# Performance work log

Hardware: AMD Instinct MI355X
Metric: run time of the kernel (lower is better)

## Reference

```python
import jax, jax.numpy as jnp
import numpy as np
from jax import lax

B, T_SRC, I, H, L, O = 1024, 1024, 64, 512, 64, 1


def _lstm_cell(x, h, c, W_ih, W_hh, b):
    # PyTorch gate order: i, f, g, o. b = b_ih + b_hh (same math).
    gates = x @ W_ih.T + h @ W_hh.T + b  # (B, 4H)
    i, f, g, o = jnp.split(gates, 4, axis=-1)
    c_new = jax.nn.sigmoid(f) * c + jax.nn.sigmoid(i) * jnp.tanh(g)
    h_new = jax.nn.sigmoid(o) * jnp.tanh(c_new)
    return h_new, c_new


def setup_inputs() -> dict:
    key = jax.random.key(0)
    ks = jax.random.split(key, 16)
    s_e = 1.0 / np.sqrt(H)
    inp = {
        "src": jax.random.normal(ks[0], (B, T_SRC, I), dtype=jnp.float32),
        "eps": jax.random.normal(ks[1], (B, L), dtype=jnp.float32),
        "tgt_len": 1024,
        # encoder LSTM
        "W_ih_e": jax.random.uniform(ks[2], (4 * H, I), jnp.float32, -s_e, s_e),
        "W_hh_e": jax.random.uniform(ks[3], (4 * H, H), jnp.float32, -s_e, s_e),
        "b_e": jax.random.uniform(ks[4], (4 * H,), jnp.float32, -s_e, s_e),
        # fc_mu / fc_logvar
        "W_mu": jax.random.uniform(ks[5], (L, H), jnp.float32, -s_e, s_e),
        "b_mu": jax.random.uniform(ks[6], (L,), jnp.float32, -s_e, s_e),
        "W_lv": jax.random.uniform(ks[7], (L, H), jnp.float32, -s_e, s_e),
        "b_lv": jax.random.uniform(ks[8], (L,), jnp.float32, -s_e, s_e),
        # z -> h0, c0
        "W_zh": jax.random.uniform(ks[9], (H, L), jnp.float32, -s_e, s_e),
        "b_zh": jax.random.uniform(ks[10], (H,), jnp.float32, -s_e, s_e),
        "W_zc": jax.random.uniform(ks[11], (H, L), jnp.float32, -s_e, s_e),
        "b_zc": jax.random.uniform(ks[12], (H,), jnp.float32, -s_e, s_e),
        # decoder LSTM + fc_out
        "W_ih_d": jax.random.uniform(ks[13], (4 * H, O), jnp.float32, -s_e, s_e),
        "W_hh_d": jax.random.uniform(ks[14], (4 * H, H), jnp.float32, -s_e, s_e),
        "b_d": jax.random.uniform(ks[15], (4 * H,), jnp.float32, -s_e, s_e),
        "W_out": jax.random.uniform(jax.random.fold_in(key, 100), (O, H), jnp.float32, -s_e, s_e),
        "b_out": jax.random.uniform(jax.random.fold_in(key, 101), (O,), jnp.float32, -s_e, s_e),
    }
    return inp


def reference(src, eps, W_ih_e, W_hh_e, b_e, W_mu, b_mu, W_lv, b_lv,
              W_zh, b_zh, W_zc, b_zc, W_ih_d, W_hh_d, b_d, W_out, b_out,
              tgt_len):
    batch = src.shape[0]
    hid = W_hh_e.shape[1]

    # ---- Encoder: LSTM over src, take final hidden state ----
    def enc_step(carry, x_t):
        h, c = carry
        h, c = _lstm_cell(x_t, h, c, W_ih_e, W_hh_e, b_e)
        return (h, c), None

    h0 = jnp.zeros((batch, hid), src.dtype)
    (h_n, _), _ = lax.scan(enc_step, (h0, h0), jnp.swapaxes(src, 0, 1))

    mu = h_n @ W_mu.T + b_mu          # (B, L)
    logvar = h_n @ W_lv.T + b_lv      # (B, L)

    # ---- Reparameterize ----
    z = mu + eps * jnp.exp(0.5 * logvar)

    h_d = jnp.tanh(z @ W_zh.T + b_zh)
    c_d = jnp.tanh(z @ W_zc.T + b_zc)
    x0 = jnp.zeros((batch, W_ih_d.shape[1]), src.dtype)  # (B, output_size)

    def dec_step(carry, _):
        h, c, x = carry
        h, c = _lstm_cell(x, h, c, W_ih_d, W_hh_d, b_d)
        out = h @ W_out.T + b_out     # (B, O)
        return (h, c, out), out

    _, outs = lax.scan(dec_step, (h_d, c_d, x0), None, length=tgt_len)
    recon = jnp.swapaxes(outs, 0, 1)  # (B, tgt_len, O)
    return recon, mu, logvar
```

## Files before the change

kernel.cpp:

```cpp
#include <hip/hip_runtime.h>


#define NWG  256
#define NTHR 256

typedef __attribute__((ext_vector_type(8))) short short8;
typedef __attribute__((ext_vector_type(4))) float f32x4;
typedef __attribute__((ext_vector_type(4))) unsigned int u32x4;

constexpr int Bt = 1024, Tt = 1024, In = 64, Hn = 512, Ln = 64;
constexpr int KE = In + Hn;
constexpr int BSE = KE + 8;
constexpr int KD = Hn;
constexpr int BSD = KD + 8;
constexpr int HSTn = 40;
constexpr int LDS_BYTES = 128 * BSE * 2 + 32 * HSTn * 2;

template<bool B> struct BoolC { static constexpr bool value = B; };

__device__ __forceinline__ float bf2f(unsigned short s){
  unsigned u = ((unsigned)s) << 16; float f; __builtin_memcpy(&f, &u, 4); return f;
}
__device__ __forceinline__ unsigned short f2bf(float f){
  unsigned u; __builtin_memcpy(&u, &f, 4);
  u += 0x7FFFu + ((u >> 16) & 1u);
  return (unsigned short)(u >> 16);
}
__device__ __forceinline__ float sigm(float x){ return 1.0f / (1.0f + __expf(-x)); }
__device__ __forceinline__ float tanh_(float x){ float e = __expf(2.0f * x); return 1.0f - 2.0f / (e + 1.0f); }

template<bool SAME, int OFF>
__device__ __forceinline__ u32x4 ldA(const void* p){
  u32x4 r;
  if constexpr (SAME) asm volatile("global_load_dwordx4 %0, %1, off offset:%c2 sc0" : "=&v"(r) : "v"(p), "i"(OFF));
  else                asm volatile("global_load_dwordx4 %0, %1, off offset:%c2 sc0 sc1" : "=&v"(r) : "v"(p), "i"(OFF));
  return r;
}
template<int OFF>
__device__ __forceinline__ u32x4 ldP(const void* p){
  u32x4 r;
  asm volatile("global_load_dwordx4 %0, %1, off offset:%c2" : "=&v"(r) : "v"(p), "i"(OFF));
  return r;
}
template<bool SAME>
__device__ __forceinline__ float ld32w(const void* p){
  float r;
  if constexpr (SAME) asm volatile("global_load_dword %0, %1, off sc0" : "=&v"(r) : "v"(p));
  else                asm volatile("global_load_dword %0, %1, off sc0 sc1" : "=&v"(r) : "v"(p));
  asm volatile("s_waitcnt vmcnt(0)" : "+v"(r));
  return r;
}
template<bool SAME>
__device__ __forceinline__ void st16x(void* p, unsigned v){
  if constexpr (SAME) asm volatile("global_store_short %0, %1, off sc0" :: "v"(p), "v"(v) : "memory");
  else                asm volatile("global_store_short %0, %1, off sc0 sc1" :: "v"(p), "v"(v) : "memory");
}
template<bool SAME>
__device__ __forceinline__ void st32x(void* p, float v){
  if constexpr (SAME) asm volatile("global_store_dword %0, %1, off sc0" :: "v"(p), "v"(v) : "memory");
  else                asm volatile("global_store_dword %0, %1, off sc0 sc1" :: "v"(p), "v"(v) : "memory");
}
template<bool SAME>
__device__ __forceinline__ void st128x(void* p, u32x4 v){
  if constexpr (SAME) asm volatile("global_store_dwordx4 %0, %1, off sc0" :: "v"(p), "v"(v) : "memory");
  else                asm volatile("global_store_dwordx4 %0, %1, off sc0 sc1" :: "v"(p), "v"(v) : "memory");
}
__device__ __forceinline__ void stP32(void* p, float v){
  asm volatile("global_store_dword %0, %1, off" :: "v"(p), "v"(v) : "memory");
}
__device__ __forceinline__ void atomAddF(float* p, float v){
  asm volatile("global_atomic_add_f32 %0, %1, off" :: "v"(p), "v"(v) : "memory");
}
__device__ __forceinline__ unsigned ldMall(const unsigned* p){
  unsigned r;
  asm volatile("global_load_dword %0, %1, off sc0 sc1" : "=&v"(r) : "v"(p) : "memory");
  asm volatile("s_waitcnt vmcnt(0)" : "+v"(r) :: "memory");
  return r;
}
__device__ __forceinline__ void stMall(unsigned* p, unsigned v){
  asm volatile("global_store_dword %0, %1, off sc0 sc1" :: "v"(p), "v"(v) : "memory");
}

__device__ __forceinline__ void release(unsigned* cnt){
  asm volatile("s_waitcnt vmcnt(0)" ::: "memory");
  __syncthreads();
  if (threadIdx.x == 0)
    __hip_atomic_fetch_add(cnt, 1u, __ATOMIC_RELAXED, __HIP_MEMORY_SCOPE_AGENT);
}
__device__ __forceinline__ void acquire(unsigned* cnt, unsigned target){
  if (threadIdx.x == 0 && target){
    int g = 0;
    while (__hip_atomic_load(cnt, __ATOMIC_RELAXED, __HIP_MEMORY_SCOPE_AGENT) < target){
      if (++g > (1 << 20)) break;
      __builtin_amdgcn_s_sleep(1);
    }
  }
  __syncthreads();
}

#define LOADC1(C, CB) do{                                  \
    A[C][0] = ldA<SAME, ((CB) +  0) * 2>(ap);              \
    A[C][1] = ldA<SAME, ((CB) + 32) * 2>(ap);              \
    A[C][2] = ldA<SAME, ((CB) + 64) * 2>(ap);              \
    A[C][3] = ldA<SAME, ((CB) + 96) * 2>(ap); }while(0)

#define TIE1(C) "+v"(A[C][0]), "+v"(A[C][1]), "+v"(A[C][2]), "+v"(A[C][3])
#define WAITC1(C, N) asm volatile("s_waitcnt vmcnt(" N ")" : TIE1(C))

#define COMPC1(C, K0, BS) do{                                                    \
    _Pragma("unroll") for (int ti_ = 0; ti_ < 4; ++ti_){                         \
      short8 a_ = __builtin_bit_cast(short8, A[C][ti_]);                         \
      _Pragma("unroll") for (int ni_ = 0; ni_ < 4; ++ni_){                       \
        short8 bv_ = *(const short8*)(bbase + ni_ * 16 * (BS) + (K0) + ti_ * 32);\
        acc[ni_] = __builtin_amdgcn_mfma_f32_16x16x32_bf16(a_, bv_, acc[ni_], 0, 0, 0); \
      } } }while(0)

extern "C" __global__ void __launch_bounds__(NTHR, 1)
vae_fused(const float* __restrict__ src, const float* __restrict__ eps,
          const float* __restrict__ Wih_e, const float* __restrict__ Whh_e, const float* __restrict__ b_e,
          const float* __restrict__ Wmu, const float* __restrict__ bmu,
          const float* __restrict__ Wlv, const float* __restrict__ blv,
          const float* __restrict__ Wzh, const float* __restrict__ bzh,
          const float* __restrict__ Wzc, const float* __restrict__ bzc,
          const float* __restrict__ Wih_d, const float* __restrict__ Whh_d, const float* __restrict__ b_d,
          const float* __restrict__ Wout, const float* __restrict__ bout,
          float* __restrict__ out,
          unsigned* cntF_all, unsigned* cntA_all, unsigned* cntB_all, unsigned* xcdbuf,
          unsigned short* hbuf0, unsigned short* hbuf1,
          float* zbuf, float* obuf)
{
  const int tid  = threadIdx.x;
  const int wg   = blockIdx.x;
  const int lane = tid & 63;
  const int wave = tid >> 6;
  const int wm   = wave >> 1, wn = wave & 1;
  const int mt   = wg & 15;
  const int nt   = wg >> 4;
  unsigned* cntF = cntF_all + mt * 16;
  unsigned* cntA = cntA_all + mt * 16;
  unsigned* cntB = cntB_all + mt * 16;
  unsigned barsF = 0;

  extern __shared__ short bpanel[];
  unsigned short* hst = (unsigned short*)(bpanel + 128 * BSE);

  const int l15 = lane & 15;
  const int l4  = lane >> 4;
  const int kq  = l4 * 8;
  const int jcol = nt * 32 + wn * 16 + l15;

  unsigned xcc;
  asm volatile("s_getreg_b32 %0, hwreg(HW_REG_XCC_ID)" : "=s"(xcc));
  if (tid == 0) stMall(xcdbuf + mt * 16 + nt, xcc + 1u);
  release(cntF); barsF += 16; acquire(cntF, barsF);
  unsigned vx = xcc + 1u;
  if (lane < 16) vx = ldMall(xcdbuf + mt * 16 + lane);
  const bool same_xcd = (__ballot(vx == xcc + 1u) == ~0ull);

  auto body = [&](auto SC){
    constexpr bool SAME = decltype(SC)::value;

    {
      const int idx = nt * NTHR + tid;
      const u32x4 z = {0u, 0u, 0u, 0u};
      st128x<SAME>(hbuf0 + (size_t)(mt * 64 + (idx >> 6)) * Hn + (idx & 63) * 8, z);
    }
    for (int idx = tid; idx < 128 * KE; idx += NTHR){
      int q = idx / KE;
      int k = idx - q * KE;
      int gate = (q >> 4) & 3, jl = q & 15, wnn = (q >> 6) & 1;
      int j = nt * 32 + wnn * 16 + jl;
      int r = gate * Hn + j;
      float w = (k < In) ? Wih_e[r * In + k] : Whh_e[(size_t)r * Hn + (k - In)];
      bpanel[q * BSE + k] = (short)f2bf(w);
    }
    float biasr[4], wihr[4];
    #pragma unroll
    for (int ni = 0; ni < 4; ++ni) biasr[ni] = b_e[ni * Hn + jcol];
    release(cntF); barsF += 16; acquire(cntF, barsF);

    float cA[4] = {0.f,0.f,0.f,0.f}, cB[4] = {0.f,0.f,0.f,0.f};
    const f32x4 fz = {0.f, 0.f, 0.f, 0.f};
    unsigned needA = 0, needB = 0;

    auto enc_phase = [&](int X, int t, unsigned* cntX, unsigned need, float (&cX)[4]){
      const int arow = mt * 64 + X * 32 + wm * 16 + l15;
      const unsigned short* hs = (t & 1) ? hbuf1 : hbuf0;
      unsigned short*       hd = (t & 1) ? hbuf0 : hbuf1;

      const float* sp = src + ((size_t)arow * Tt + t) * In + kq;
      u32x4 sv0 = ldP<0>(sp), sv1 = ldP<16>(sp), sv2 = ldP<128>(sp), sv3 = ldP<144>(sp);

      acquire(cntX, need);

      const unsigned short* ap = hs + (size_t)arow * Hn + kq;
      u32x4 A[4][4];
      LOADC1(0,   0); LOADC1(1, 128); LOADC1(2, 256); LOADC1(3, 384);

      asm volatile("s_waitcnt vmcnt(16)" : "+v"(sv0), "+v"(sv1), "+v"(sv2), "+v"(sv3));
      f32x4 f0 = __builtin_bit_cast(f32x4, sv0);
      f32x4 f1 = __builtin_bit_cast(f32x4, sv1);
      f32x4 f2 = __builtin_bit_cast(f32x4, sv2);
      f32x4 f3 = __builtin_bit_cast(f32x4, sv3);
      short8 sa0, sa1;
      #pragma unroll
      for (int e = 0; e < 4; ++e){
        sa0[e] = (short)f2bf(f0[e]); sa0[4 + e] = (short)f2bf(f1[e]);
        sa1[e] = (short)f2bf(f2[e]); sa1[4 + e] = (short)f2bf(f3[e]);
      }

      f32x4 acc[4] = {fz, fz, fz, fz};
      const short* bbase = bpanel + (wn * 64 + l15) * BSE + kq;
      #pragma unroll
      for (int ni = 0; ni < 4; ++ni){
        short8 bv0 = *(const short8*)(bbase + ni * 16 * BSE + 0);
        short8 bv1 = *(const short8*)(bbase + ni * 16 * BSE + 32);
        acc[ni] = __builtin_amdgcn_mfma_f32_16x16x32_bf16(sa0, bv0, acc[ni], 0, 0, 0);
        acc[ni] = __builtin_amdgcn_mfma_f32_16x16x32_bf16(sa1, bv1, acc[ni], 0, 0, 0);
      }

      WAITC1(0, "12"); COMPC1(0, In +   0, BSE);
      WAITC1(1,  "8"); COMPC1(1, In + 128, BSE);
      WAITC1(2,  "4"); COMPC1(2, In + 256, BSE);
      WAITC1(3,  "0"); COMPC1(3, In + 384, BSE);

      #pragma unroll
      for (int r = 0; r < 4; ++r){
        float gi = acc[0][r] + biasr[0];
        float gf = acc[1][r] + biasr[1];
        float gg = acc[2][r] + biasr[2];
        float go = acc[3][r] + biasr[3];
        float cn = sigm(gf) * cX[r] + sigm(gi) * tanh_(gg);
        cX[r] = cn;
        float hn = sigm(go) * tanh_(cn);
        hst[(wm * 16 + l4 * 4 + r) * HSTn + wn * 16 + l15] = f2bf(hn);
      }
      __syncthreads();
      if (tid < 128){
        u32x4 hv = *(const u32x4*)(hst + (tid >> 2) * HSTn + (tid & 3) * 8);
        st128x<SAME>(hd + (size_t)(mt * 64 + X * 32 + (tid >> 2)) * Hn + nt * 32 + (tid & 3) * 8, hv);
      }
      release(cntX);
    };

    for (int t = 0; t < Tt; ++t){
      enc_phase(0, t, cntA, needA, cA); needA += 16;
      enc_phase(1, t, cntB, needB, cB); needB += 16;
    }
    release(cntF); barsF += 16; acquire(cntF, barsF);

    {
      const int lt = nt * NTHR + tid;
      const int b  = mt * 64 + (lt >> 6);
      const int l  = lt & 63;
      const unsigned short* hp = hbuf0 + (size_t)b * Hn;
      const float* wmrow = Wmu + l * Hn;
      const float* wlrow = Wlv + l * Hn;
      float smu = 0.f, slv = 0.f;
      for (int jj = 0; jj < Hn; jj += 32){
        u32x4 v0 = ldA<SAME,0>(hp + jj),  v1 = ldA<SAME,16>(hp + jj);
        u32x4 v2 = ldA<SAME,32>(hp + jj), v3 = ldA<SAME,48>(hp + jj);
        asm volatile("s_waitcnt vmcnt(0)" : "+v"(v0), "+v"(v1), "+v"(v2), "+v"(v3));
        short8 h0 = __builtin_bit_cast(short8, v0);
        short8 h1 = __builtin_bit_cast(short8, v1);
        short8 h2 = __builtin_bit_cast(short8, v2);
        short8 h3 = __builtin_bit_cast(short8, v3);
        #pragma unroll
        for (int e = 0; e < 8; ++e){
          float g0 = bf2f((unsigned short)h0[e]), g1 = bf2f((unsigned short)h1[e]);
          float g2 = bf2f((unsigned short)h2[e]), g3 = bf2f((unsigned short)h3[e]);
          smu = __builtin_fmaf(g0, wmrow[jj + e], smu);      slv = __builtin_fmaf(g0, wlrow[jj + e], slv);
          smu = __builtin_fmaf(g1, wmrow[jj + 8 + e], smu);  slv = __builtin_fmaf(g1, wlrow[jj + 8 + e], slv);
          smu = __builtin_fmaf(g2, wmrow[jj + 16 + e], smu); slv = __builtin_fmaf(g2, wlrow[jj + 16 + e], slv);
          smu = __builtin_fmaf(g3, wmrow[jj + 24 + e], smu); slv = __builtin_fmaf(g3, wlrow[jj + 24 + e], slv);
        }
      }
      smu += bmu[l]; slv += blv[l];
      out[(size_t)Bt * Tt + (size_t)b * Ln + l] = smu;
      out[(size_t)Bt * Tt + (size_t)Bt * Ln + (size_t)b * Ln + l] = slv;
      st32x<SAME>(zbuf + (size_t)b * Ln + l, smu + eps[(size_t)b * Ln + l] * __expf(0.5f * slv));
    }
    release(cntF); barsF += 16; acquire(cntF, barsF);

    for (int idx = tid; idx < 128 * KD; idx += NTHR){
      int q = idx >> 9, k = idx & 511;
      int gate = (q >> 4) & 3, jl = q & 15, wnn = (q >> 6) & 1;
      int j = nt * 32 + wnn * 16 + jl;
      bpanel[q * BSD + k] = (short)f2bf(Whh_d[(size_t)(gate * Hn + j) * Hn + k]);
    }
    #pragma unroll
    for (int ni = 0; ni < 4; ++ni){
      biasr[ni] = b_d[ni * Hn + jcol];
      wihr[ni]  = Wih_d[ni * Hn + jcol];
    }
    const float woutr = Wout[jcol];
    const float bov   = bout[0];

    auto dec_init = [&](int X, float (&cX)[4]){
      #pragma unroll
      for (int r = 0; r < 4; ++r){
        int b = mt * 64 + X * 32 + wm * 16 + l4 * 4 + r;
        const float* zp  = zbuf + (size_t)b * Ln;
        const float* whr = Wzh + jcol * Ln;
        const float* wcr = Wzc + jcol * Ln;
        float sh = bzh[jcol], sc = bzc[jcol];
        for (int e0 = 0; e0 < Ln; e0 += 16){
          u32x4 z0 = ldA<SAME,0>(zp + e0),  z1 = ldA<SAME,16>(zp + e0);
          u32x4 z2 = ldA<SAME,32>(zp + e0), z3 = ldA<SAME,48>(zp + e0);
          asm volatile("s_waitcnt vmcnt(0)" : "+v"(z0), "+v"(z1), "+v"(z2), "+v"(z3));
          f32x4 zf0 = __builtin_bit_cast(f32x4, z0);
          f32x4 zf1 = __builtin_bit_cast(f32x4, z1);
          f32x4 zf2 = __builtin_bit_cast(f32x4, z2);
          f32x4 zf3 = __builtin_bit_cast(f32x4, z3);
          #pragma unroll
          for (int e = 0; e < 4; ++e){
            sh = __builtin_fmaf(zf0[e], whr[e0 + e], sh);      sc = __builtin_fmaf(zf0[e], wcr[e0 + e], sc);
            sh = __builtin_fmaf(zf1[e], whr[e0 + 4 + e], sh);  sc = __builtin_fmaf(zf1[e], wcr[e0 + 4 + e], sc);
            sh = __builtin_fmaf(zf2[e], whr[e0 + 8 + e], sh);  sc = __builtin_fmaf(zf2[e], wcr[e0 + 8 + e], sc);
            sh = __builtin_fmaf(zf3[e], whr[e0 + 12 + e], sh); sc = __builtin_fmaf(zf3[e], wcr[e0 + 12 + e], sc);
          }
        }
        cX[r] = tanh_(sc);
        st16x<SAME>(hbuf0 + (size_t)b * Hn + jcol, (unsigned)f2bf(tanh_(sh)));
      }
    };
    dec_init(0, cA);
    dec_init(1, cB);
    if (nt == 0 && tid < 3 * 64)
      st32x<SAME>(obuf + (tid >> 6) * Bt + mt * 64 + (tid & 63), bov);
    release(cntF); barsF += 16; acquire(cntF, barsF);

    auto dec_phase = [&](int X, int t, unsigned* cntX, unsigned need, float (&cX)[4]){
      const int arow = mt * 64 + X * 32 + wm * 16 + l15;
      const int brow = mt * 64 + X * 32 + wm * 16 + l4 * 4;
      const int rX0  = mt * 64 + X * 32;
      const unsigned short* hs = (t & 1) ? hbuf1 : hbuf0;
      unsigned short*       hd = (t & 1) ? hbuf0 : hbuf1;
      float*       oacc  = obuf + (t % 3) * Bt;
      const float* oread = obuf + ((t + 2) % 3) * Bt;
      float*       orst  = obuf + ((t + 1) % 3) * Bt;

      acquire(cntX, need);

      if (nt == 0){
        if (t > 0 && tid < 32){
          float w = ld32w<SAME>(oread + rX0 + tid);
          stP32(out + (size_t)(rX0 + tid) * Tt + (t - 1), w);
        }
        if (tid < 32) st32x<SAME>(orst + rX0 + tid, bov);
      }

      u32x4 xvv = ldA<SAME, 0>(oread + brow);
      const unsigned short* ap = hs + (size_t)arow * Hn + kq;
      u32x4 A[4][4];
      LOADC1(0,   0); LOADC1(1, 128); LOADC1(2, 256); LOADC1(3, 384);

      f32x4 acc[4] = {fz, fz, fz, fz};
      const short* bbase = bpanel + (wn * 64 + l15) * BSD + kq;
      WAITC1(0, "12"); COMPC1(0,   0, BSD);
      WAITC1(1,  "8"); COMPC1(1, 128, BSD);
      WAITC1(2,  "4"); COMPC1(2, 256, BSD);
      WAITC1(3,  "0"); COMPC1(3, 384, BSD);
      asm volatile("s_waitcnt vmcnt(0)" : "+v"(xvv));
      f32x4 xf = __builtin_bit_cast(f32x4, xvv);

      #pragma unroll
      for (int r = 0; r < 4; ++r){
        float x = (t == 0) ? 0.f : xf[r];
        float gi = acc[0][r] + biasr[0] + x * wihr[0];
        float gf = acc[1][r] + biasr[1] + x * wihr[1];
        float gg = acc[2][r] + biasr[2] + x * wihr[2];
        float go = acc[3][r] + biasr[3] + x * wihr[3];
        float cn = sigm(gf) * cX[r] + sigm(gi) * tanh_(gg);
        cX[r] = cn;
        float hn = sigm(go) * tanh_(cn);
        hst[(wm * 16 + l4 * 4 + r) * HSTn + wn * 16 + l15] = f2bf(hn);
        float pv = hn * woutr;
        pv += __shfl_xor(pv, 1);
        pv += __shfl_xor(pv, 2);
        pv += __shfl_xor(pv, 4);
        pv += __shfl_xor(pv, 8);
        if (l15 == 0) atomAddF(&oacc[brow + r], pv);
      }
      __syncthreads();
      if (tid < 128){
        u32x4 hv = *(const u32x4*)(hst + (tid >> 2) * HSTn + (tid & 3) * 8);
        st128x<SAME>(hd + (size_t)(mt * 64 + X * 32 + (tid >> 2)) * Hn + nt * 32 + (tid & 3) * 8, hv);
      }
      release(cntX);
    };

    for (int t = 0; t < Tt; ++t){
      dec_phase(0, t, cntA, needA, cA); needA += 16;
      dec_phase(1, t, cntB, needB, cB); needB += 16;
    }
    release(cntF); barsF += 16; acquire(cntF, barsF);

    if (nt == 0 && tid < 64){
      float w = ld32w<SAME>(obuf + 0 * Bt + mt * 64 + tid);
      stP32(out + (size_t)(mt * 64 + tid) * Tt + (Tt - 1), w);
    }
  };

  if (same_xcd) body(BoolC<true>{});
  else          body(BoolC<false>{});
}

extern "C" void kernel_launch(void* const* d_in, const int* in_sizes, int n_in,
                              void* d_out, int out_size, void* d_ws, size_t ws_size,
                              hipStream_t stream){
  (void)in_sizes; (void)n_in; (void)out_size; (void)ws_size;
  const float* src   = (const float*)d_in[0];
  const float* eps   = (const float*)d_in[1];
  const float* Wih_e = (const float*)d_in[3];
  const float* Whh_e = (const float*)d_in[4];
  const float* b_e   = (const float*)d_in[5];
  const float* Wmu   = (const float*)d_in[6];
  const float* bmu   = (const float*)d_in[7];
  const float* Wlv   = (const float*)d_in[8];
  const float* blv   = (const float*)d_in[9];
  const float* Wzh   = (const float*)d_in[10];
  const float* bzh   = (const float*)d_in[11];
  const float* Wzc   = (const float*)d_in[12];
  const float* bzc   = (const float*)d_in[13];
  const float* Wih_d = (const float*)d_in[14];
  const float* Whh_d = (const float*)d_in[15];
  const float* b_d   = (const float*)d_in[16];
  const float* Wout  = (const float*)d_in[17];
  const float* bout  = (const float*)d_in[18];

  char* ws = (char*)d_ws;
  unsigned*       cntF  = (unsigned*)ws;
  unsigned*       cntA  = (unsigned*)(ws + 1024);
  unsigned*       cntB  = (unsigned*)(ws + 2048);
  unsigned*       xcdb  = (unsigned*)(ws + 3072);
  unsigned short* h0    = (unsigned short*)(ws + 4096);
  unsigned short* h1    = (unsigned short*)(ws + 4096 + 1048576);
  float*          zbuf  = (float*)(ws + 4096 + 2 * 1048576);
  float*          obuf  = (float*)(ws + 4096 + 2 * 1048576 + 262144);

  hipFuncSetAttribute((const void*)vae_fused,
                      hipFuncAttributeMaxDynamicSharedMemorySize, LDS_BYTES);
  (void)hipMemsetAsync(ws, 0, 4096, stream);
  hipLaunchKernelGGL(vae_fused, dim3(NWG), dim3(NTHR), LDS_BYTES, stream,
                     src, eps, Wih_e, Whh_e, b_e, Wmu, bmu, Wlv, blv,
                     Wzh, bzh, Wzc, bzc, Wih_d, Whh_d, b_d, Wout, bout,
                     (float*)d_out, cntF, cntA, cntB, xcdb, h0, h1, zbuf, obuf);
}
```

Baseline: 17.93 ms.

## Double block size to process both 32-row halves concurrently with one barrier per step

Workgroups grow from 256 to 512 threads, so the 8 waves cover all 64 batch rows of a tile in one pass instead of alternating two 32-row halves with separate counters. Each timestep now does a single group barrier over one counter rather than two split-phase acquire/release pairs, and the spin-wait timeout is dropped. The decoder's float atomic add also gets an sc1 variant when the group spans XCDs. The cost is that the old overlap between one half's compute and the other half's barrier wait is lost. Register pressure per thread also rises under the new launch bounds.

```diff
diff --git a/kernel.cpp b/kernel.cpp
--- a/kernel.cpp
+++ b/kernel.cpp
@@ -2,7 +2,7 @@
 
 
 #define NWG  256
-#define NTHR 256
+#define NTHR 512
 
 typedef __attribute__((ext_vector_type(8))) short short8;
 typedef __attribute__((ext_vector_type(4))) float f32x4;
@@ -13,8 +13,8 @@
 constexpr int BSE = KE + 8;
 constexpr int KD = Hn;
 constexpr int BSD = KD + 8;
-constexpr int HSTn = 40;
-constexpr int LDS_BYTES = 128 * BSE * 2 + 32 * HSTn * 2;
+constexpr int HST = 40;
+constexpr int LDS_BYTES = 128 * BSE * 2 + 64 * HST * 2;
 
 template<bool B> struct BoolC { static constexpr bool value = B; };
 
@@ -68,8 +68,10 @@
 __device__ __forceinline__ void stP32(void* p, float v){
   asm volatile("global_store_dword %0, %1, off" :: "v"(p), "v"(v) : "memory");
 }
+template<bool SAME>
 __device__ __forceinline__ void atomAddF(float* p, float v){
-  asm volatile("global_atomic_add_f32 %0, %1, off" :: "v"(p), "v"(v) : "memory");
+  if constexpr (SAME) asm volatile("global_atomic_add_f32 %0, %1, off" :: "v"(p), "v"(v) : "memory");
+  else                asm volatile("global_atomic_add_f32 %0, %1, off sc1" :: "v"(p), "v"(v) : "memory");
 }
 __device__ __forceinline__ unsigned ldMall(const unsigned* p){
   unsigned r;
@@ -81,19 +83,13 @@
   asm volatile("global_store_dword %0, %1, off sc0 sc1" :: "v"(p), "v"(v) : "memory");
 }
 
-__device__ __forceinline__ void release(unsigned* cnt){
+__device__ __forceinline__ void group_sync(unsigned* cnt, unsigned target){
   asm volatile("s_waitcnt vmcnt(0)" ::: "memory");
   __syncthreads();
-  if (threadIdx.x == 0)
+  if (threadIdx.x == 0){
     __hip_atomic_fetch_add(cnt, 1u, __ATOMIC_RELAXED, __HIP_MEMORY_SCOPE_AGENT);
-}
-__device__ __forceinline__ void acquire(unsigned* cnt, unsigned target){
-  if (threadIdx.x == 0 && target){
-    int g = 0;
-    while (__hip_atomic_load(cnt, __ATOMIC_RELAXED, __HIP_MEMORY_SCOPE_AGENT) < target){
-      if (++g > (1 << 20)) break;
+    while (__hip_atomic_load(cnt, __ATOMIC_RELAXED, __HIP_MEMORY_SCOPE_AGENT) < target)
       __builtin_amdgcn_s_sleep(1);
-    }
   }
   __syncthreads();
 }
@@ -115,7 +111,7 @@
         acc[ni_] = __builtin_amdgcn_mfma_f32_16x16x32_bf16(a_, bv_, acc[ni_], 0, 0, 0); \
       } } }while(0)
 
-extern "C" __global__ void __launch_bounds__(NTHR, 1)
+extern "C" __global__ void __launch_bounds__(NTHR, 2)
 vae_fused(const float* __restrict__ src, const float* __restrict__ eps,
           const float* __restrict__ Wih_e, const float* __restrict__ Whh_e, const float* __restrict__ b_e,
           const float* __restrict__ Wmu, const float* __restrict__ bmu,
@@ -125,7 +121,7 @@
           const float* __restrict__ Wih_d, const float* __restrict__ Whh_d, const float* __restrict__ b_d,
           const float* __restrict__ Wout, const float* __restrict__ bout,
           float* __restrict__ out,
-          unsigned* cntF_all, unsigned* cntA_all, unsigned* cntB_all, unsigned* xcdbuf,
+          unsigned* cnt_all, unsigned* xcdbuf,
           unsigned short* hbuf0, unsigned short* hbuf1,
           float* zbuf, float* obuf)
 {
@@ -133,26 +129,27 @@
   const int wg   = blockIdx.x;
   const int lane = tid & 63;
   const int wave = tid >> 6;
-  const int wm   = wave >> 1, wn = wave & 1;
+  const int wm   = wave >> 1;
+  const int wn   = wave & 1;
   const int mt   = wg & 15;
   const int nt   = wg >> 4;
-  unsigned* cntF = cntF_all + mt * 16;
-  unsigned* cntA = cntA_all + mt * 16;
-  unsigned* cntB = cntB_all + mt * 16;
-  unsigned barsF = 0;
+  unsigned* cnt  = cnt_all + mt * 32;
+  unsigned bars  = 0;
 
   extern __shared__ short bpanel[];
   unsigned short* hst = (unsigned short*)(bpanel + 128 * BSE);
 
-  const int l15 = lane & 15;
-  const int l4  = lane >> 4;
-  const int kq  = l4 * 8;
-  const int jcol = nt * 32 + wn * 16 + l15;
+  const int l15   = lane & 15;
+  const int l4    = lane >> 4;
+  const int kq    = l4 * 8;
+  const int jcol  = nt * 32 + wn * 16 + l15;
+  const int arow0 = mt * 64 + wm * 16 + l15;
+  const int brow0 = mt * 64 + wm * 16 + l4 * 4;
 
   unsigned xcc;
   asm volatile("s_getreg_b32 %0, hwreg(HW_REG_XCC_ID)" : "=s"(xcc));
   if (tid == 0) stMall(xcdbuf + mt * 16 + nt, xcc + 1u);
-  release(cntF); barsF += 16; acquire(cntF, barsF);
+  bars += 16; group_sync(cnt, bars);
   unsigned vx = xcc + 1u;
   if (lane < 16) vx = ldMall(xcdbuf + mt * 16 + lane);
   const bool same_xcd = (__ballot(vx == xcc + 1u) == ~0ull);
@@ -162,8 +159,10 @@
 
     {
       const int idx = nt * NTHR + tid;
-      const u32x4 z = {0u, 0u, 0u, 0u};
-      st128x<SAME>(hbuf0 + (size_t)(mt * 64 + (idx >> 6)) * Hn + (idx & 63) * 8, z);
+      if (idx < 4096){
+        const u32x4 z = {0u, 0u, 0u, 0u};
+        st128x<SAME>(hbuf0 + (size_t)(mt * 64 + (idx >> 6)) * Hn + (idx & 63) * 8, z);
+      }
     }
     for (int idx = tid; idx < 128 * KE; idx += NTHR){
       int q = idx / KE;
@@ -177,24 +176,20 @@
     float biasr[4], wihr[4];
     #pragma unroll
     for (int ni = 0; ni < 4; ++ni) biasr[ni] = b_e[ni * Hn + jcol];
-    release(cntF); barsF += 16; acquire(cntF, barsF);
-
-    float cA[4] = {0.f,0.f,0.f,0.f}, cB[4] = {0.f,0.f,0.f,0.f};
+    bars += 16; group_sync(cnt, bars);
+
+    float c[4] = {0.f, 0.f, 0.f, 0.f};
     const f32x4 fz = {0.f, 0.f, 0.f, 0.f};
-    unsigned needA = 0, needB = 0;
-
-    auto enc_phase = [&](int X, int t, unsigned* cntX, unsigned need, float (&cX)[4]){
-      const int arow = mt * 64 + X * 32 + wm * 16 + l15;
+    u32x4 A[4][4];
+
+    for (int t = 0; t < Tt; ++t){
       const unsigned short* hs = (t & 1) ? hbuf1 : hbuf0;
       unsigned short*       hd = (t & 1) ? hbuf0 : hbuf1;
 
-      const float* sp = src + ((size_t)arow * Tt + t) * In + kq;
+      const float* sp = src + ((size_t)arow0 * Tt + t) * In + kq;
       u32x4 sv0 = ldP<0>(sp), sv1 = ldP<16>(sp), sv2 = ldP<128>(sp), sv3 = ldP<144>(sp);
 
-      acquire(cntX, need);
-
-      const unsigned short* ap = hs + (size_t)arow * Hn + kq;
-      u32x4 A[4][4];
+      const unsigned short* ap = hs + (size_t)arow0 * Hn + kq;
       LOADC1(0,   0); LOADC1(1, 128); LOADC1(2, 256); LOADC1(3, 384);
 
       asm volatile("s_waitcnt vmcnt(16)" : "+v"(sv0), "+v"(sv1), "+v"(sv2), "+v"(sv3));
@@ -230,57 +225,54 @@
         float gf = acc[1][r] + biasr[1];
         float gg = acc[2][r] + biasr[2];
         float go = acc[3][r] + biasr[3];
-        float cn = sigm(gf) * cX[r] + sigm(gi) * tanh_(gg);
-        cX[r] = cn;
+        float cn = sigm(gf) * c[r] + sigm(gi) * tanh_(gg);
+        c[r] = cn;
         float hn = sigm(go) * tanh_(cn);
-        hst[(wm * 16 + l4 * 4 + r) * HSTn + wn * 16 + l15] = f2bf(hn);
+        hst[(wm * 16 + l4 * 4 + r) * HST + wn * 16 + l15] = f2bf(hn);
       }
       __syncthreads();
-      if (tid < 128){
-        u32x4 hv = *(const u32x4*)(hst + (tid >> 2) * HSTn + (tid & 3) * 8);
-        st128x<SAME>(hd + (size_t)(mt * 64 + X * 32 + (tid >> 2)) * Hn + nt * 32 + (tid & 3) * 8, hv);
-      }
-      release(cntX);
-    };
-
-    for (int t = 0; t < Tt; ++t){
-      enc_phase(0, t, cntA, needA, cA); needA += 16;
-      enc_phase(1, t, cntB, needB, cB); needB += 16;
-    }
-    release(cntF); barsF += 16; acquire(cntF, barsF);
+      if (tid < 256){
+        int row = tid >> 2, sub = tid & 3;
+        u32x4 hv = *(const u32x4*)(hst + row * HST + sub * 8);
+        st128x<SAME>(hd + (size_t)(mt * 64 + row) * Hn + nt * 32 + sub * 8, hv);
+      }
+      bars += 16; group_sync(cnt, bars);
+    }
 
     {
       const int lt = nt * NTHR + tid;
-      const int b  = mt * 64 + (lt >> 6);
-      const int l  = lt & 63;
-      const unsigned short* hp = hbuf0 + (size_t)b * Hn;
-      const float* wmrow = Wmu + l * Hn;
-      const float* wlrow = Wlv + l * Hn;
-      float smu = 0.f, slv = 0.f;
-      for (int jj = 0; jj < Hn; jj += 32){
-        u32x4 v0 = ldA<SAME,0>(hp + jj),  v1 = ldA<SAME,16>(hp + jj);
-        u32x4 v2 = ldA<SAME,32>(hp + jj), v3 = ldA<SAME,48>(hp + jj);
-        asm volatile("s_waitcnt vmcnt(0)" : "+v"(v0), "+v"(v1), "+v"(v2), "+v"(v3));
-        short8 h0 = __builtin_bit_cast(short8, v0);
-        short8 h1 = __builtin_bit_cast(short8, v1);
-        short8 h2 = __builtin_bit_cast(short8, v2);
-        short8 h3 = __builtin_bit_cast(short8, v3);
-        #pragma unroll
-        for (int e = 0; e < 8; ++e){
-          float g0 = bf2f((unsigned short)h0[e]), g1 = bf2f((unsigned short)h1[e]);
-          float g2 = bf2f((unsigned short)h2[e]), g3 = bf2f((unsigned short)h3[e]);
-          smu = __builtin_fmaf(g0, wmrow[jj + e], smu);      slv = __builtin_fmaf(g0, wlrow[jj + e], slv);
-          smu = __builtin_fmaf(g1, wmrow[jj + 8 + e], smu);  slv = __builtin_fmaf(g1, wlrow[jj + 8 + e], slv);
-          smu = __builtin_fmaf(g2, wmrow[jj + 16 + e], smu); slv = __builtin_fmaf(g2, wlrow[jj + 16 + e], slv);
-          smu = __builtin_fmaf(g3, wmrow[jj + 24 + e], smu); slv = __builtin_fmaf(g3, wlrow[jj + 24 + e], slv);
+      if (lt < 4096){
+        const int b  = mt * 64 + (lt >> 6);
+        const int l  = lt & 63;
+        const unsigned short* hp = hbuf0 + (size_t)b * Hn;
+        const float* wmrow = Wmu + l * Hn;
+        const float* wlrow = Wlv + l * Hn;
+        float smu = 0.f, slv = 0.f;
+        for (int jj = 0; jj < Hn; jj += 32){
+          u32x4 v0 = ldA<SAME,0>(hp + jj),  v1 = ldA<SAME,16>(hp + jj);
+          u32x4 v2 = ldA<SAME,32>(hp + jj), v3 = ldA<SAME,48>(hp + jj);
+          asm volatile("s_waitcnt vmcnt(0)" : "+v"(v0), "+v"(v1), "+v"(v2), "+v"(v3));
+          short8 h0 = __builtin_bit_cast(short8, v0);
+          short8 h1 = __builtin_bit_cast(short8, v1);
+          short8 h2 = __builtin_bit_cast(short8, v2);
+          short8 h3 = __builtin_bit_cast(short8, v3);
+          #pragma unroll
+          for (int e = 0; e < 8; ++e){
+            float g0 = bf2f((unsigned short)h0[e]), g1 = bf2f((unsigned short)h1[e]);
+            float g2 = bf2f((unsigned short)h2[e]), g3 = bf2f((unsigned short)h3[e]);
+            smu = __builtin_fmaf(g0, wmrow[jj + e], smu);      slv = __builtin_fmaf(g0, wlrow[jj + e], slv);
+            smu = __builtin_fmaf(g1, wmrow[jj + 8 + e], smu);  slv = __builtin_fmaf(g1, wlrow[jj + 8 + e], slv);
+            smu = __builtin_fmaf(g2, wmrow[jj + 16 + e], smu); slv = __builtin_fmaf(g2, wlrow[jj + 16 + e], slv);
+            smu = __builtin_fmaf(g3, wmrow[jj + 24 + e], smu); slv = __builtin_fmaf(g3, wlrow[jj + 24 + e], slv);
+          }
         }
-      }
-      smu += bmu[l]; slv += blv[l];
-      out[(size_t)Bt * Tt + (size_t)b * Ln + l] = smu;
-      out[(size_t)Bt * Tt + (size_t)Bt * Ln + (size_t)b * Ln + l] = slv;
-      st32x<SAME>(zbuf + (size_t)b * Ln + l, smu + eps[(size_t)b * Ln + l] * __expf(0.5f * slv));
-    }
-    release(cntF); barsF += 16; acquire(cntF, barsF);
+        smu += bmu[l]; slv += blv[l];
+        out[(size_t)Bt * Tt + (size_t)b * Ln + l] = smu;
+        out[(size_t)Bt * Tt + (size_t)Bt * Ln + (size_t)b * Ln + l] = slv;
+        st32x<SAME>(zbuf + (size_t)b * Ln + l, smu + eps[(size_t)b * Ln + l] * __expf(0.5f * slv));
+      }
+    }
+    bars += 16; group_sync(cnt, bars);
 
     for (int idx = tid; idx < 128 * KD; idx += NTHR){
       int q = idx >> 9, k = idx & 511;
@@ -295,64 +287,53 @@
     }
     const float woutr = Wout[jcol];
     const float bov   = bout[0];
-
-    auto dec_init = [&](int X, float (&cX)[4]){
-      #pragma unroll
-      for (int r = 0; r < 4; ++r){
-        int b = mt * 64 + X * 32 + wm * 16 + l4 * 4 + r;
-        const float* zp  = zbuf + (size_t)b * Ln;
-        const float* whr = Wzh + jcol * Ln;
-        const float* wcr = Wzc + jcol * Ln;
-        float sh = bzh[jcol], sc = bzc[jcol];
-        for (int e0 = 0; e0 < Ln; e0 += 16){
-          u32x4 z0 = ldA<SAME,0>(zp + e0),  z1 = ldA<SAME,16>(zp + e0);
-          u32x4 z2 = ldA<SAME,32>(zp + e0), z3 = ldA<SAME,48>(zp + e0);
-          asm volatile("s_waitcnt vmcnt(0)" : "+v"(z0), "+v"(z1), "+v"(z2), "+v"(z3));
-          f32x4 zf0 = __builtin_bit_cast(f32x4, z0);
-          f32x4 zf1 = __builtin_bit_cast(f32x4, z1);
-          f32x4 zf2 = __builtin_bit_cast(f32x4, z2);
-          f32x4 zf3 = __builtin_bit_cast(f32x4, z3);
-          #pragma unroll
-          for (int e = 0; e < 4; ++e){
-            sh = __builtin_fmaf(zf0[e], whr[e0 + e], sh);      sc = __builtin_fmaf(zf0[e], wcr[e0 + e], sc);
-            sh = __builtin_fmaf(zf1[e], whr[e0 + 4 + e], sh);  sc = __builtin_fmaf(zf1[e], wcr[e0 + 4 + e], sc);
-            sh = __builtin_fmaf(zf2[e], whr[e0 + 8 + e], sh);  sc = __builtin_fmaf(zf2[e], wcr[e0 + 8 + e], sc);
-            sh = __builtin_fmaf(zf3[e], whr[e0 + 12 + e], sh); sc = __builtin_fmaf(zf3[e], wcr[e0 + 12 + e], sc);
-          }
+    #pragma unroll
+    for (int r = 0; r < 4; ++r){
+      int b = brow0 + r;
+      const float* zp  = zbuf + (size_t)b * Ln;
+      const float* whr = Wzh + jcol * Ln;
+      const float* wcr = Wzc + jcol * Ln;
+      float sh = bzh[jcol], sc = bzc[jcol];
+      for (int e0 = 0; e0 < Ln; e0 += 16){
+        u32x4 z0 = ldA<SAME,0>(zp + e0),  z1 = ldA<SAME,16>(zp + e0);
+        u32x4 z2 = ldA<SAME,32>(zp + e0), z3 = ldA<SAME,48>(zp + e0);
+        asm volatile("s_waitcnt vmcnt(0)" : "+v"(z0), "+v"(z1), "+v"(z2), "+v"(z3));
+        f32x4 zf0 = __builtin_bit_cast(f32x4, z0);
+        f32x4 zf1 = __builtin_bit_cast(f32x4, z1);
+        f32x4 zf2 = __builtin_bit_cast(f32x4, z2);
+        f32x4 zf3 = __builtin_bit_cast(f32x4, z3);
+        #pragma unroll
+        for (int e = 0; e < 4; ++e){
+          sh = __builtin_fmaf(zf0[e], whr[e0 + e], sh);      sc = __builtin_fmaf(zf0[e], wcr[e0 + e], sc);
+          sh = __builtin_fmaf(zf1[e], whr[e0 + 4 + e], sh);  sc = __builtin_fmaf(zf1[e], wcr[e0 + 4 + e], sc);
+          sh = __builtin_fmaf(zf2[e], whr[e0 + 8 + e], sh);  sc = __builtin_fmaf(zf2[e], wcr[e0 + 8 + e], sc);
+          sh = __builtin_fmaf(zf3[e], whr[e0 + 12 + e], sh); sc = __builtin_fmaf(zf3[e], wcr[e0 + 12 + e], sc);
         }
-        cX[r] = tanh_(sc);
-        st16x<SAME>(hbuf0 + (size_t)b * Hn + jcol, (unsigned)f2bf(tanh_(sh)));
-      }
-    };
-    dec_init(0, cA);
-    dec_init(1, cB);
+      }
+      c[r] = tanh_(sc);
+      st16x<SAME>(hbuf0 + (size_t)b * Hn + jcol, (unsigned)f2bf(tanh_(sh)));
+    }
     if (nt == 0 && tid < 3 * 64)
       st32x<SAME>(obuf + (tid >> 6) * Bt + mt * 64 + (tid & 63), bov);
-    release(cntF); barsF += 16; acquire(cntF, barsF);
-
-    auto dec_phase = [&](int X, int t, unsigned* cntX, unsigned need, float (&cX)[4]){
-      const int arow = mt * 64 + X * 32 + wm * 16 + l15;
-      const int brow = mt * 64 + X * 32 + wm * 16 + l4 * 4;
-      const int rX0  = mt * 64 + X * 32;
+    bars += 16; group_sync(cnt, bars);
+
+    for (int t = 0; t < Tt; ++t){
       const unsigned short* hs = (t & 1) ? hbuf1 : hbuf0;
       unsigned short*       hd = (t & 1) ? hbuf0 : hbuf1;
       float*       oacc  = obuf + (t % 3) * Bt;
       const float* oread = obuf + ((t + 2) % 3) * Bt;
       float*       orst  = obuf + ((t + 1) % 3) * Bt;
 
-      acquire(cntX, need);
-
       if (nt == 0){
-        if (t > 0 && tid < 32){
-          float w = ld32w<SAME>(oread + rX0 + tid);
-          stP32(out + (size_t)(rX0 + tid) * Tt + (t - 1), w);
+        if (t > 0 && tid < 64){
+          float w = ld32w<SAME>(oread + mt * 64 + tid);
+          stP32(out + (size_t)(mt * 64 + tid) * Tt + (t - 1), w);
         }
-        if (tid < 32) st32x<SAME>(orst + rX0 + tid, bov);
-      }
-
-      u32x4 xvv = ldA<SAME, 0>(oread + brow);
-      const unsigned short* ap = hs + (size_t)arow * Hn + kq;
-      u32x4 A[4][4];
+        if (tid < 64) st32x<SAME>(orst + mt * 64 + tid, bov);
+      }
+
+      u32x4 xvv = ldA<SAME, 0>(oread + brow0);
+      const unsigned short* ap = hs + (size_t)arow0 * Hn + kq;
       LOADC1(0,   0); LOADC1(1, 128); LOADC1(2, 256); LOADC1(3, 384);
 
       f32x4 acc[4] = {fz, fz, fz, fz};
@@ -371,31 +352,25 @@
         float gf = acc[1][r] + biasr[1] + x * wihr[1];
         float gg = acc[2][r] + biasr[2] + x * wihr[2];
         float go = acc[3][r] + biasr[3] + x * wihr[3];
-        float cn = sigm(gf) * cX[r] + sigm(gi) * tanh_(gg);
-        cX[r] = cn;
+        float cn = sigm(gf) * c[r] + sigm(gi) * tanh_(gg);
+        c[r] = cn;
         float hn = sigm(go) * tanh_(cn);
-        hst[(wm * 16 + l4 * 4 + r) * HSTn + wn * 16 + l15] = f2bf(hn);
+        hst[(wm * 16 + l4 * 4 + r) * HST + wn * 16 + l15] = f2bf(hn);
         float pv = hn * woutr;
         pv += __shfl_xor(pv, 1);
         pv += __shfl_xor(pv, 2);
         pv += __shfl_xor(pv, 4);
         pv += __shfl_xor(pv, 8);
-        if (l15 == 0) atomAddF(&oacc[brow + r], pv);
+        if (l15 == 0) atomAddF<SAME>(&oacc[brow0 + r], pv);
       }
       __syncthreads();
-      if (tid < 128){
-        u32x4 hv = *(const u32x4*)(hst + (tid >> 2) * HSTn + (tid & 3) * 8);
-        st128x<SAME>(hd + (size_t)(mt * 64 + X * 32 + (tid >> 2)) * Hn + nt * 32 + (tid & 3) * 8, hv);
-      }
-      release(cntX);
-    };
-
-    for (int t = 0; t < Tt; ++t){
-      dec_phase(0, t, cntA, needA, cA); needA += 16;
-      dec_phase(1, t, cntB, needB, cB); needB += 16;
-    }
-    release(cntF); barsF += 16; acquire(cntF, barsF);
-
+      if (tid < 256){
+        int row = tid >> 2, sub = tid & 3;
+        u32x4 hv = *(const u32x4*)(hst + row * HST + sub * 8);
+        st128x<SAME>(hd + (size_t)(mt * 64 + row) * Hn + nt * 32 + sub * 8, hv);
+      }
+      bars += 16; group_sync(cnt, bars);
+    }
     if (nt == 0 && tid < 64){
       float w = ld32w<SAME>(obuf + 0 * Bt + mt * 64 + tid);
       stP32(out + (size_t)(mt * 64 + tid) * Tt + (Tt - 1), w);
@@ -430,10 +405,8 @@
   const float* bout  = (const float*)d_in[18];
 
   char* ws = (char*)d_ws;
-  unsigned*       cntF  = (unsigned*)ws;
-  unsigned*       cntA  = (unsigned*)(ws + 1024);
-  unsigned*       cntB  = (unsigned*)(ws + 2048);
-  unsigned*       xcdb  = (unsigned*)(ws + 3072);
+  unsigned*       cnt   = (unsigned*)ws;
+  unsigned*       xcdb  = (unsigned*)(ws + 2048);
   unsigned short* h0    = (unsigned short*)(ws + 4096);
   unsigned short* h1    = (unsigned short*)(ws + 4096 + 1048576);
   float*          zbuf  = (float*)(ws + 4096 + 2 * 1048576);
@@ -445,5 +418,5 @@
   hipLaunchKernelGGL(vae_fused, dim3(NWG), dim3(NTHR), LDS_BYTES, stream,
                      src, eps, Wih_e, Whh_e, b_e, Wmu, bmu, Wlv, blv,
                      Wzh, bzh, Wzc, bzc, Wih_d, Whh_d, b_d, Wout, bout,
-                     (float*)d_out, cntF, cntA, cntB, xcdb, h0, h1, zbuf, obuf);
-}
+                     (float*)d_out, cnt, xcdb, h0, h1, zbuf, obuf);
+}
```

Measured after the change: 15.04 ms (median of 2 runs). 1.19x faster.
